# Performance work log

Measured on AMD Instinct MI355X. Metric: run time of the kernel, lower is better.

The kernel has to match this reference:

```python
import jax, jax.numpy as jnp
import numpy as np

N, E, D, H = 8192, 8, 2048, 2048


def setup_inputs() -> dict:
    key = jax.random.key(0)
    k1, k2, k3, k4 = jax.random.split(key, 4)
    x = jax.random.normal(k1, (N, D), dtype=jnp.float32)
    indices = jax.random.randint(k2, (N, 1), 0, E)  # top_k=1 expert assignment
    W = jax.random.normal(k3, (E, D, H), dtype=jnp.float32) * 0.02
    b = jax.random.normal(k4, (E, H), dtype=jnp.float32) * 0.02
    return {"x": x, "indices": indices, "W": W, "b": b}


def reference(x, indices, W, b):
    # Each token is routed to exactly one expert (top_k=1):
    # expert_id[n] = indices[n, 0]. The torch module loops experts e=0..E-1,
    # gathers tokens with (indices == e).any(-1) (ascending order via nonzero),
    # applies expert e's Linear + ReLU, and concatenates outputs in expert order.
    expert_id = indices[:, 0]                              # [N]
    # Dense dispatch: compute every expert's linear on every token, then pick
    # each token's own expert row (jit-friendly; no data-dependent shapes).
    y_all = jnp.einsum('nd,edh->neh', x, W) + b[None, :, :]  # [N, E, H]
    y = jnp.take_along_axis(y_all, expert_id[:, None, None], axis=1)[:, 1 - 1, :]  # [N, H]
    y = jax.nn.relu(y)
    # Concat in expert order == stable sort of tokens by expert id
    # (nonzero returns ascending indices, so within-expert order is preserved).
    order = jnp.argsort(expert_id)  # stable by default
    return y[order]
```

## Files before the change

kernel.cpp:

```cpp
#include <hip/hip_runtime.h>

#define N_TOK 8192
#define N_EXP 8
#define DIM   2048
#define HID   2048

typedef __attribute__((ext_vector_type(8))) short short8;
typedef __attribute__((ext_vector_type(4))) float f32x4;
typedef __attribute__((ext_vector_type(4))) unsigned short ushort4v;

__device__ inline unsigned short f2bf(float f) {
  unsigned int u = __builtin_bit_cast(unsigned int, f);
  unsigned int r = u + 0x7FFFu + ((u >> 16) & 1u);
  return (unsigned short)(r >> 16);
}

__global__ __launch_bounds__(256) void sort_experts(const int* __restrict__ idx,
                                                    int* __restrict__ perm,
                                                    int* __restrict__ offs) {
  __shared__ int cnt[256][8];
  __shared__ int base[8];
  const int t = threadIdx.x;
  int local[8] = {0,0,0,0,0,0,0,0};
  const int r0 = t * 32;
  for (int i = 0; i < 32; ++i) {
    int e = idx[r0 + i] & 7;
    ++local[e];
  }
#pragma unroll
  for (int e = 0; e < 8; ++e) cnt[t][e] = local[e];
  __syncthreads();
  if (t < 8) {
    int s = 0;
    for (int i = 0; i < 256; ++i) { int v = cnt[i][t]; cnt[i][t] = s; s += v; }
    base[t] = s;
  }
  __syncthreads();
  if (t == 0) {
    int s = 0;
    for (int e = 0; e < 8; ++e) { int v = base[e]; offs[e] = s; base[e] = s; s += v; }
    offs[8] = s;
  }
  __syncthreads();
  int pos[8];
#pragma unroll
  for (int e = 0; e < 8; ++e) pos[e] = base[e] + cnt[t][e];
  for (int i = 0; i < 32; ++i) {
    int r = r0 + i;
    int e = idx[r] & 7;
    perm[pos[e]++] = r;
  }
}

__global__ __launch_bounds__(256) void gather_convert_x(const float* __restrict__ x,
                                                        const int* __restrict__ perm,
                                                        unsigned short* __restrict__ xs) {
  int gid = blockIdx.x * 256 + threadIdx.x;
  int p = gid >> 8;
  int c = gid & 255;
  int src = perm[p];
  const float* sp = x + (size_t)src * DIM + c * 8;
  float4 a = *(const float4*)sp;
  float4 b = *(const float4*)(sp + 4);
  short8 o;
  o[0] = (short)f2bf(a.x); o[1] = (short)f2bf(a.y);
  o[2] = (short)f2bf(a.z); o[3] = (short)f2bf(a.w);
  o[4] = (short)f2bf(b.x); o[5] = (short)f2bf(b.y);
  o[6] = (short)f2bf(b.z); o[7] = (short)f2bf(b.w);
  *(short8*)(xs + (size_t)p * DIM + c * 8) = o;
}

__global__ __launch_bounds__(256) void transpose_convert_w(const float* __restrict__ W,
                                                           unsigned short* __restrict__ Wt) {
  __shared__ unsigned short tile[64][68];
  const int e = blockIdx.z;
  const int d0 = blockIdx.y * 64;
  const int h0 = blockIdx.x * 64;
  const int t = threadIdx.x;
  const int cr = t & 15;
  const int rr = t >> 4;
  const float* Wp = W + ((size_t)e * DIM + d0) * HID + h0;
#pragma unroll
  for (int i = 0; i < 4; ++i) {
    int d = rr + i * 16;
    float4 v = *(const float4*)(Wp + (size_t)d * HID + cr * 4);
    ushort4v o;
    o[0] = f2bf(v.x); o[1] = f2bf(v.y); o[2] = f2bf(v.z); o[3] = f2bf(v.w);
    *(ushort4v*)&tile[d][cr * 4] = o;
  }
  __syncthreads();
  unsigned short* op = Wt + ((size_t)e * HID + h0) * DIM + d0;
#pragma unroll
  for (int i = 0; i < 4; ++i) {
    int h = rr + i * 16;
    ushort4v o;
    o[0] = tile[cr * 4 + 0][h];
    o[1] = tile[cr * 4 + 1][h];
    o[2] = tile[cr * 4 + 2][h];
    o[3] = tile[cr * 4 + 3][h];
    *(ushort4v*)(op + (size_t)h * DIM + cr * 4) = o;
  }
}

#define NKT 32
#define SLOT_USH 24576

#define MM(D,A,B) D = __builtin_amdgcn_mfma_f32_16x16x32_bf16(A, B, D, 0, 0, 0)
#define GLD(SRC, DST) __builtin_amdgcn_global_load_lds( \
    (const __attribute__((address_space(1))) void*)(SRC), \
    (__attribute__((address_space(3))) void*)(DST), 16, 0, 0)
#define BAR() __builtin_amdgcn_s_barrier()
#define PRIO(x) __builtin_amdgcn_s_setprio(x)

__global__ __launch_bounds__(512, 2) void grouped_gemm(
    const unsigned short* __restrict__ xs,
    const unsigned short* __restrict__ Wt,
    const float* __restrict__ bias,
    const int* __restrict__ offs,
    float* __restrict__ out) {
  const int e   = blockIdx.z;
  const int off = offs[e];
  const int cnt = offs[e + 1] - off;
  const int mt  = blockIdx.y;
  if (mt * 128 >= cnt) return;
  const int n0 = blockIdx.x * 256;

  __shared__ __align__(16) unsigned short sm[3 * SLOT_USH];

  const int t    = threadIdx.x;
  const int lane = t & 63;
  const int wid  = t >> 6;
  const int wr   = wid >> 2;
  const int wc   = wid & 3;
  const int l15  = lane & 15;
  const int l4   = lane >> 4;

  const int cb0  = (l4 * 8) ^ ((l15 & 7) << 3);
  const int cb1  = cb0 ^ 32;
  const int arow = (wr * 64 + l15) * 64;
  const int brow = 8192 + (wc * 64 + l15) * 64;

  const int r0  = t >> 3;
  const int keu = ((t & 7) * 8) ^ ((r0 & 7) << 3);
  const int aBase = off + mt * 128;
  const int dA = t * 8;

  unsigned int pa0, pa1, pb0, pb1, pb2, pb3;
  {
    int p;
    p = aBase + 0 * 64 + r0; if (p > N_TOK - 1) p = N_TOK - 1; pa0 = (unsigned)p * 2048 + keu;
    p = aBase + 1 * 64 + r0; if (p > N_TOK - 1) p = N_TOK - 1; pa1 = (unsigned)p * 2048 + keu;
    unsigned int eW = (unsigned)e * (DIM * HID);
    pb0 = eW + (unsigned)(n0 + 0 * 64 + r0) * 2048 + keu;
    pb1 = eW + (unsigned)(n0 + 1 * 64 + r0) * 2048 + keu;
    pb2 = eW + (unsigned)(n0 + 2 * 64 + r0) * 2048 + keu;
    pb3 = eW + (unsigned)(n0 + 3 * 64 + r0) * 2048 + keu;
  }

#define ST_A(SBASE, KOFS) do { \
    GLD(xs + pa0 + (KOFS), sm + (SBASE) + 0 * 4096 + dA); \
    GLD(xs + pa1 + (KOFS), sm + (SBASE) + 1 * 4096 + dA); } while (0)
#define ST_B0(SBASE, KOFS) GLD(Wt + pb0 + (KOFS), sm + (SBASE) + 8192 + 0 * 4096 + dA)
#define ST_B123(SBASE, KOFS) do { \
    GLD(Wt + pb1 + (KOFS), sm + (SBASE) + 8192 + 1 * 4096 + dA); \
    GLD(Wt + pb2 + (KOFS), sm + (SBASE) + 8192 + 2 * 4096 + dA); \
    GLD(Wt + pb3 + (KOFS), sm + (SBASE) + 8192 + 3 * 4096 + dA); } while (0)

#define READ_FRAGS(SP, CB) \
    fa0 = *(const short8*)((SP) + arow + 0 * 1024 + (CB)); \
    fa1 = *(const short8*)((SP) + arow + 1 * 1024 + (CB)); \
    fa2 = *(const short8*)((SP) + arow + 2 * 1024 + (CB)); \
    fa3 = *(const short8*)((SP) + arow + 3 * 1024 + (CB)); \
    fb0 = *(const short8*)((SP) + brow + 0 * 1024 + (CB)); \
    fb1 = *(const short8*)((SP) + brow + 1 * 1024 + (CB)); \
    fb2 = *(const short8*)((SP) + brow + 2 * 1024 + (CB)); \
    fb3 = *(const short8*)((SP) + brow + 3 * 1024 + (CB));

#define MFMA16() \
    MM(acc[0][0],fa0,fb0); MM(acc[0][1],fa0,fb1); MM(acc[0][2],fa0,fb2); MM(acc[0][3],fa0,fb3); \
    MM(acc[1][0],fa1,fb0); MM(acc[1][1],fa1,fb1); MM(acc[1][2],fa1,fb2); MM(acc[1][3],fa1,fb3); \
    MM(acc[2][0],fa2,fb0); MM(acc[2][1],fa2,fb1); MM(acc[2][2],fa2,fb2); MM(acc[2][3],fa2,fb3); \
    MM(acc[3][0],fa3,fb0); MM(acc[3][1],fa3,fb1); MM(acc[3][2],fa3,fb2); MM(acc[3][3],fa3,fb3);

  f32x4 acc[4][4] = {};

  ST_A(0, 0); ST_B0(0, 0); ST_B123(0, 0);
  ST_A(SLOT_USH, 64); ST_B0(SLOT_USH, 64); ST_B123(SLOT_USH, 64);
  asm volatile("s_waitcnt vmcnt(6)" ::: "memory");
  BAR();

  short8 fa0, fa1, fa2, fa3, fb0, fb1, fb2, fb3;
  int sl = 0;
  int s2 = 2;

#pragma unroll 1
  for (int T = 0; T < NKT; ++T) {
    const unsigned short* SP = sm + sl * SLOT_USH;
    const int sb = s2 * SLOT_USH;
    const int kofs = (T + 2) * 64;
    const bool st = (T < NKT - 2);

    READ_FRAGS(SP, cb0);
    if (st) { ST_A(sb, kofs); ST_B0(sb, kofs); }
    BAR(); PRIO(1);
    MFMA16();
    PRIO(0); BAR();

    READ_FRAGS(SP, cb1);
    if (st) { ST_B123(sb, kofs); }
    BAR(); PRIO(1);
    MFMA16();
    PRIO(0);
    if (T < NKT - 2)       { asm volatile("s_waitcnt vmcnt(6)" ::: "memory"); }
    else if (T == NKT - 2) { asm volatile("s_waitcnt vmcnt(0)" ::: "memory"); }
    BAR();

    sl = (sl == 2) ? 0 : sl + 1;
    s2 = (s2 == 2) ? 0 : s2 + 1;
  }

#pragma unroll
  for (int n = 0; n < 4; ++n) {
    int col = n0 + wc * 64 + n * 16 + l15;
    float bv = bias[e * HID + col];
#pragma unroll
    for (int m = 0; m < 4; ++m) {
#pragma unroll
      for (int q = 0; q < 4; ++q) {
        int r = wr * 64 + m * 16 + l4 * 4 + q;
        if (mt * 128 + r < cnt) {
          float v = acc[m][n][q] + bv;
          out[(size_t)(off + mt * 128 + r) * HID + col] = v > 0.f ? v : 0.f;
        }
      }
    }
  }
}

extern "C" void kernel_launch(void* const* d_in, const int* in_sizes, int n_in,
                              void* d_out, int out_size, void* d_ws, size_t ws_size,
                              hipStream_t stream) {
  const float* x   = (const float*)d_in[0];
  const int*   idx = (const int*)d_in[1];
  const float* W   = (const float*)d_in[2];
  const float* b   = (const float*)d_in[3];
  float* out = (float*)d_out;

  char* ws = (char*)d_ws;
  unsigned short* xs = (unsigned short*)ws;
  unsigned short* Wt = (unsigned short*)(ws + (size_t)N_TOK * DIM * 2);
  int* perm = (int*)(ws + (size_t)N_TOK * DIM * 2 + (size_t)N_EXP * DIM * HID * 2);
  int* offs = perm + N_TOK;

  sort_experts<<<1, 256, 0, stream>>>(idx, perm, offs);
  gather_convert_x<<<N_TOK * (DIM / 8) / 256, 256, 0, stream>>>(x, perm, xs);
  transpose_convert_w<<<dim3(HID / 64, DIM / 64, N_EXP), 256, 0, stream>>>(W, Wt);
  grouped_gemm<<<dim3(HID / 256, N_TOK / 128, N_EXP), 512, 0, stream>>>(xs, Wt, b, offs, out);
}
```

Measured before the change: 182.6 us.

## Shrink GEMM tile to 128x128 with K=32 steps and 4-stage pipeline

Changes the grouped GEMM block tile from 128x256 with 512 threads to 128x128 with 256 threads, cutting each K step from 64 to 32 and moving from a 3-slot to a 4-slot LDS ring that loads three tiles ahead. The LDS swizzle and per-step load and MFMA schedule are rewritten to match. The aim is more blocks for better CU occupancy and less LDS per block. The cost is lower arithmetic intensity per loaded byte and twice as many barriers per K.

```diff
diff --git a/kernel.cpp b/kernel.cpp
--- a/kernel.cpp
+++ b/kernel.cpp
@@ -102,8 +102,8 @@
   }
 }
 
-#define NKT 32
-#define SLOT_USH 24576
+#define NKT 64
+#define SLOT 8192
 
 #define MM(D,A,B) D = __builtin_amdgcn_mfma_f32_16x16x32_bf16(A, B, D, 0, 0, 0)
 #define GLD(SRC, DST) __builtin_amdgcn_global_load_lds( \
@@ -112,7 +112,7 @@
 #define BAR() __builtin_amdgcn_s_barrier()
 #define PRIO(x) __builtin_amdgcn_s_setprio(x)
 
-__global__ __launch_bounds__(512, 2) void grouped_gemm(
+__global__ __launch_bounds__(256, 2) void grouped_gemm(
     const unsigned short* __restrict__ xs,
     const unsigned short* __restrict__ Wt,
     const float* __restrict__ bias,
@@ -123,29 +123,28 @@
   const int cnt = offs[e + 1] - off;
   const int mt  = blockIdx.y;
   if (mt * 128 >= cnt) return;
-  const int n0 = blockIdx.x * 256;
-
-  __shared__ __align__(16) unsigned short sm[3 * SLOT_USH];
+  const int n0 = blockIdx.x * 128;
+
+  __shared__ __align__(16) unsigned short sm[4 * SLOT];
 
   const int t    = threadIdx.x;
   const int lane = t & 63;
   const int wid  = t >> 6;
-  const int wr   = wid >> 2;
-  const int wc   = wid & 3;
+  const int wr   = wid >> 1;
+  const int wc   = wid & 1;
   const int l15  = lane & 15;
   const int l4   = lane >> 4;
 
-  const int cb0  = (l4 * 8) ^ ((l15 & 7) << 3);
-  const int cb1  = cb0 ^ 32;
-  const int arow = (wr * 64 + l15) * 64;
-  const int brow = 8192 + (wc * 64 + l15) * 64;
-
-  const int r0  = t >> 3;
-  const int keu = ((t & 7) * 8) ^ ((r0 & 7) << 3);
+  const int ksw = (l4 ^ (l15 & 3)) * 8;
+  const int arow = (wr * 64 + l15) * 32;
+  const int brow = 4096 + (wc * 64 + l15) * 32;
+
+  const int r0  = t >> 2;
+  const int keu = ((t & 3) ^ (r0 & 3)) * 8;
   const int aBase = off + mt * 128;
   const int dA = t * 8;
 
-  unsigned int pa0, pa1, pb0, pb1, pb2, pb3;
+  unsigned int pa0, pa1, pb0, pb1;
   {
     int p;
     p = aBase + 0 * 64 + r0; if (p > N_TOK - 1) p = N_TOK - 1; pa0 = (unsigned)p * 2048 + keu;
@@ -153,70 +152,49 @@
     unsigned int eW = (unsigned)e * (DIM * HID);
     pb0 = eW + (unsigned)(n0 + 0 * 64 + r0) * 2048 + keu;
     pb1 = eW + (unsigned)(n0 + 1 * 64 + r0) * 2048 + keu;
-    pb2 = eW + (unsigned)(n0 + 2 * 64 + r0) * 2048 + keu;
-    pb3 = eW + (unsigned)(n0 + 3 * 64 + r0) * 2048 + keu;
-  }
-
-#define ST_A(SBASE, KOFS) do { \
-    GLD(xs + pa0 + (KOFS), sm + (SBASE) + 0 * 4096 + dA); \
-    GLD(xs + pa1 + (KOFS), sm + (SBASE) + 1 * 4096 + dA); } while (0)
-#define ST_B0(SBASE, KOFS) GLD(Wt + pb0 + (KOFS), sm + (SBASE) + 8192 + 0 * 4096 + dA)
-#define ST_B123(SBASE, KOFS) do { \
-    GLD(Wt + pb1 + (KOFS), sm + (SBASE) + 8192 + 1 * 4096 + dA); \
-    GLD(Wt + pb2 + (KOFS), sm + (SBASE) + 8192 + 2 * 4096 + dA); \
-    GLD(Wt + pb3 + (KOFS), sm + (SBASE) + 8192 + 3 * 4096 + dA); } while (0)
-
-#define READ_FRAGS(SP, CB) \
-    fa0 = *(const short8*)((SP) + arow + 0 * 1024 + (CB)); \
-    fa1 = *(const short8*)((SP) + arow + 1 * 1024 + (CB)); \
-    fa2 = *(const short8*)((SP) + arow + 2 * 1024 + (CB)); \
-    fa3 = *(const short8*)((SP) + arow + 3 * 1024 + (CB)); \
-    fb0 = *(const short8*)((SP) + brow + 0 * 1024 + (CB)); \
-    fb1 = *(const short8*)((SP) + brow + 1 * 1024 + (CB)); \
-    fb2 = *(const short8*)((SP) + brow + 2 * 1024 + (CB)); \
-    fb3 = *(const short8*)((SP) + brow + 3 * 1024 + (CB));
-
-#define MFMA16() \
-    MM(acc[0][0],fa0,fb0); MM(acc[0][1],fa0,fb1); MM(acc[0][2],fa0,fb2); MM(acc[0][3],fa0,fb3); \
-    MM(acc[1][0],fa1,fb0); MM(acc[1][1],fa1,fb1); MM(acc[1][2],fa1,fb2); MM(acc[1][3],fa1,fb3); \
-    MM(acc[2][0],fa2,fb0); MM(acc[2][1],fa2,fb1); MM(acc[2][2],fa2,fb2); MM(acc[2][3],fa2,fb3); \
-    MM(acc[3][0],fa3,fb0); MM(acc[3][1],fa3,fb1); MM(acc[3][2],fa3,fb2); MM(acc[3][3],fa3,fb3);
+  }
+
+#define ST_TILE(SBASE, KOFS) do { \
+    GLD(xs + pa0 + (KOFS), sm + (SBASE) + 0 * 2048 + dA); \
+    GLD(xs + pa1 + (KOFS), sm + (SBASE) + 1 * 2048 + dA); \
+    GLD(Wt + pb0 + (KOFS), sm + (SBASE) + 4096 + 0 * 2048 + dA); \
+    GLD(Wt + pb1 + (KOFS), sm + (SBASE) + 4096 + 1 * 2048 + dA); } while (0)
 
   f32x4 acc[4][4] = {};
 
-  ST_A(0, 0); ST_B0(0, 0); ST_B123(0, 0);
-  ST_A(SLOT_USH, 64); ST_B0(SLOT_USH, 64); ST_B123(SLOT_USH, 64);
-  asm volatile("s_waitcnt vmcnt(6)" ::: "memory");
+  ST_TILE(0 * SLOT, 0);
+  ST_TILE(1 * SLOT, 32);
+  ST_TILE(2 * SLOT, 64);
+  asm volatile("s_waitcnt vmcnt(8)" ::: "memory");
   BAR();
 
   short8 fa0, fa1, fa2, fa3, fb0, fb1, fb2, fb3;
-  int sl = 0;
-  int s2 = 2;
 
 #pragma unroll 1
   for (int T = 0; T < NKT; ++T) {
-    const unsigned short* SP = sm + sl * SLOT_USH;
-    const int sb = s2 * SLOT_USH;
-    const int kofs = (T + 2) * 64;
-    const bool st = (T < NKT - 2);
-
-    READ_FRAGS(SP, cb0);
-    if (st) { ST_A(sb, kofs); ST_B0(sb, kofs); }
+    const unsigned short* SP = sm + (T & 3) * SLOT;
+
+    fa0 = *(const short8*)(SP + arow + 0 * 512 + ksw);
+    fa1 = *(const short8*)(SP + arow + 1 * 512 + ksw);
+    fa2 = *(const short8*)(SP + arow + 2 * 512 + ksw);
+    fa3 = *(const short8*)(SP + arow + 3 * 512 + ksw);
+    fb0 = *(const short8*)(SP + brow + 0 * 512 + ksw);
+    fb1 = *(const short8*)(SP + brow + 1 * 512 + ksw);
+    fb2 = *(const short8*)(SP + brow + 2 * 512 + ksw);
+    fb3 = *(const short8*)(SP + brow + 3 * 512 + ksw);
+
+    if (T < NKT - 3) ST_TILE(((T + 3) & 3) * SLOT, (T + 3) * 32);
+
     BAR(); PRIO(1);
-    MFMA16();
-    PRIO(0); BAR();
-
-    READ_FRAGS(SP, cb1);
-    if (st) { ST_B123(sb, kofs); }
-    BAR(); PRIO(1);
-    MFMA16();
+    MM(acc[0][0],fa0,fb0); MM(acc[0][1],fa0,fb1); MM(acc[0][2],fa0,fb2); MM(acc[0][3],fa0,fb3);
+    MM(acc[1][0],fa1,fb0); MM(acc[1][1],fa1,fb1); MM(acc[1][2],fa1,fb2); MM(acc[1][3],fa1,fb3);
+    MM(acc[2][0],fa2,fb0); MM(acc[2][1],fa2,fb1); MM(acc[2][2],fa2,fb2); MM(acc[2][3],fa2,fb3);
+    MM(acc[3][0],fa3,fb0); MM(acc[3][1],fa3,fb1); MM(acc[3][2],fa3,fb2); MM(acc[3][3],fa3,fb3);
     PRIO(0);
-    if (T < NKT - 2)       { asm volatile("s_waitcnt vmcnt(6)" ::: "memory"); }
+    if (T < NKT - 3)       { asm volatile("s_waitcnt vmcnt(8)" ::: "memory"); }
+    else if (T == NKT - 3) { asm volatile("s_waitcnt vmcnt(4)" ::: "memory"); }
     else if (T == NKT - 2) { asm volatile("s_waitcnt vmcnt(0)" ::: "memory"); }
     BAR();
-
-    sl = (sl == 2) ? 0 : sl + 1;
-    s2 = (s2 == 2) ? 0 : s2 + 1;
   }
 
 #pragma unroll
@@ -255,5 +233,5 @@
   sort_experts<<<1, 256, 0, stream>>>(idx, perm, offs);
   gather_convert_x<<<N_TOK * (DIM / 8) / 256, 256, 0, stream>>>(x, perm, xs);
   transpose_convert_w<<<dim3(HID / 64, DIM / 64, N_EXP), 256, 0, stream>>>(W, Wt);
-  grouped_gemm<<<dim3(HID / 256, N_TOK / 128, N_EXP), 512, 0, stream>>>(xs, Wt, b, offs, out);
-}
+  grouped_gemm<<<dim3(HID / 128, N_TOK / 128, N_EXP), 256, 0, stream>>>(xs, Wt, b, offs, out);
+}
```

Result: no change. 184.4 us (+1.0%).

## Use persistent job-list grouped GEMM with 256x128 tiles and merge prep kernels

Applied to the files above, without the earlier changes.

The sort kernel now also builds a compact list of (expert, m-tile) jobs, so the GEMM becomes a persistent 256-block kernel that loops only over real tiles instead of launching a full grid where many blocks exit early. The block tile changes from 128x256 to 256x128 (2x4 waves become 4x2), which alters the load split across the two half-stages. The x gather/convert and W transpose/convert kernels are merged into one launch to save a launch and let the two overlap. Risks include tail imbalance from the fixed 256-block stride and the extra indirection through the job list.

```diff
diff --git a/kernel.cpp b/kernel.cpp
--- a/kernel.cpp
+++ b/kernel.cpp
@@ -17,7 +17,8 @@
 
 __global__ __launch_bounds__(256) void sort_experts(const int* __restrict__ idx,
                                                     int* __restrict__ perm,
-                                                    int* __restrict__ offs) {
+                                                    int* __restrict__ offs,
+                                                    int* __restrict__ jobs) {
   __shared__ int cnt[256][8];
   __shared__ int base[8];
   const int t = threadIdx.x;
@@ -37,9 +38,15 @@
   }
   __syncthreads();
   if (t == 0) {
-    int s = 0;
-    for (int e = 0; e < 8; ++e) { int v = base[e]; offs[e] = s; base[e] = s; s += v; }
+    int s = 0, njm = 0;
+    for (int e = 0; e < 8; ++e) {
+      int v = base[e];
+      offs[e] = s; base[e] = s; s += v;
+      int nm = (v + 255) >> 8;
+      for (int mt = 0; mt < nm; ++mt) jobs[1 + njm++] = e | (mt << 8);
+    }
     offs[8] = s;
+    jobs[0] = njm;
   }
   __syncthreads();
   int pos[8];
@@ -52,58 +59,60 @@
   }
 }
 
-__global__ __launch_bounds__(256) void gather_convert_x(const float* __restrict__ x,
-                                                        const int* __restrict__ perm,
-                                                        unsigned short* __restrict__ xs) {
-  int gid = blockIdx.x * 256 + threadIdx.x;
-  int p = gid >> 8;
-  int c = gid & 255;
-  int src = perm[p];
-  const float* sp = x + (size_t)src * DIM + c * 8;
-  float4 a = *(const float4*)sp;
-  float4 b = *(const float4*)(sp + 4);
-  short8 o;
-  o[0] = (short)f2bf(a.x); o[1] = (short)f2bf(a.y);
-  o[2] = (short)f2bf(a.z); o[3] = (short)f2bf(a.w);
-  o[4] = (short)f2bf(b.x); o[5] = (short)f2bf(b.y);
-  o[6] = (short)f2bf(b.z); o[7] = (short)f2bf(b.w);
-  *(short8*)(xs + (size_t)p * DIM + c * 8) = o;
-}
-
-__global__ __launch_bounds__(256) void transpose_convert_w(const float* __restrict__ W,
-                                                           unsigned short* __restrict__ Wt) {
+__global__ __launch_bounds__(256) void prep(const float* __restrict__ x,
+                                            const int* __restrict__ perm,
+                                            unsigned short* __restrict__ xs,
+                                            const float* __restrict__ W,
+                                            unsigned short* __restrict__ Wt) {
   __shared__ unsigned short tile[64][68];
-  const int e = blockIdx.z;
-  const int d0 = blockIdx.y * 64;
-  const int h0 = blockIdx.x * 64;
   const int t = threadIdx.x;
-  const int cr = t & 15;
-  const int rr = t >> 4;
-  const float* Wp = W + ((size_t)e * DIM + d0) * HID + h0;
-#pragma unroll
-  for (int i = 0; i < 4; ++i) {
-    int d = rr + i * 16;
-    float4 v = *(const float4*)(Wp + (size_t)d * HID + cr * 4);
-    ushort4v o;
-    o[0] = f2bf(v.x); o[1] = f2bf(v.y); o[2] = f2bf(v.z); o[3] = f2bf(v.w);
-    *(ushort4v*)&tile[d][cr * 4] = o;
-  }
-  __syncthreads();
-  unsigned short* op = Wt + ((size_t)e * HID + h0) * DIM + d0;
-#pragma unroll
-  for (int i = 0; i < 4; ++i) {
-    int h = rr + i * 16;
-    ushort4v o;
-    o[0] = tile[cr * 4 + 0][h];
-    o[1] = tile[cr * 4 + 1][h];
-    o[2] = tile[cr * 4 + 2][h];
-    o[3] = tile[cr * 4 + 3][h];
-    *(ushort4v*)(op + (size_t)h * DIM + cr * 4) = o;
+  if (blockIdx.x < 8192) {
+    int gid = blockIdx.x * 256 + t;
+    int p = gid >> 8;
+    int c = gid & 255;
+    int src = perm[p];
+    const float* sp = x + (size_t)src * DIM + c * 8;
+    float4 a = *(const float4*)sp;
+    float4 b = *(const float4*)(sp + 4);
+    short8 o;
+    o[0] = (short)f2bf(a.x); o[1] = (short)f2bf(a.y);
+    o[2] = (short)f2bf(a.z); o[3] = (short)f2bf(a.w);
+    o[4] = (short)f2bf(b.x); o[5] = (short)f2bf(b.y);
+    o[6] = (short)f2bf(b.z); o[7] = (short)f2bf(b.w);
+    *(short8*)(xs + (size_t)p * DIM + c * 8) = o;
+  } else {
+    const int b = blockIdx.x - 8192;
+    const int e  = b >> 10;
+    const int d0 = ((b >> 5) & 31) * 64;
+    const int h0 = (b & 31) * 64;
+    const int cr = t & 15;
+    const int rr = t >> 4;
+    const float* Wp = W + ((size_t)e * DIM + d0) * HID + h0;
+#pragma unroll
+    for (int i = 0; i < 4; ++i) {
+      int d = rr + i * 16;
+      float4 v = *(const float4*)(Wp + (size_t)d * HID + cr * 4);
+      ushort4v o;
+      o[0] = f2bf(v.x); o[1] = f2bf(v.y); o[2] = f2bf(v.z); o[3] = f2bf(v.w);
+      *(ushort4v*)&tile[d][cr * 4] = o;
+    }
+    __syncthreads();
+    unsigned short* op = Wt + ((size_t)e * HID + h0) * DIM + d0;
+#pragma unroll
+    for (int i = 0; i < 4; ++i) {
+      int h = rr + i * 16;
+      ushort4v o;
+      o[0] = tile[cr * 4 + 0][h];
+      o[1] = tile[cr * 4 + 1][h];
+      o[2] = tile[cr * 4 + 2][h];
+      o[3] = tile[cr * 4 + 3][h];
+      *(ushort4v*)(op + (size_t)h * DIM + cr * 4) = o;
+    }
   }
 }
 
 #define NKT 32
-#define SLOT_USH 24576
+#define SLOT 24576
 
 #define MM(D,A,B) D = __builtin_amdgcn_mfma_f32_16x16x32_bf16(A, B, D, 0, 0, 0)
 #define GLD(SRC, DST) __builtin_amdgcn_global_load_lds( \
@@ -117,124 +126,138 @@
     const unsigned short* __restrict__ Wt,
     const float* __restrict__ bias,
     const int* __restrict__ offs,
+    const int* __restrict__ jobs,
     float* __restrict__ out) {
-  const int e   = blockIdx.z;
-  const int off = offs[e];
-  const int cnt = offs[e + 1] - off;
-  const int mt  = blockIdx.y;
-  if (mt * 128 >= cnt) return;
-  const int n0 = blockIdx.x * 256;
-
-  __shared__ __align__(16) unsigned short sm[3 * SLOT_USH];
+  __shared__ __align__(16) unsigned short sm[3 * SLOT];
 
   const int t    = threadIdx.x;
   const int lane = t & 63;
   const int wid  = t >> 6;
-  const int wr   = wid >> 2;
-  const int wc   = wid & 3;
+  const int wr   = wid >> 1;
+  const int wc   = wid & 1;
   const int l15  = lane & 15;
   const int l4   = lane >> 4;
 
   const int cb0  = (l4 * 8) ^ ((l15 & 7) << 3);
   const int cb1  = cb0 ^ 32;
   const int arow = (wr * 64 + l15) * 64;
-  const int brow = 8192 + (wc * 64 + l15) * 64;
+  const int brow = 16384 + (wc * 64 + l15) * 64;
 
   const int r0  = t >> 3;
   const int keu = ((t & 7) * 8) ^ ((r0 & 7) << 3);
-  const int aBase = off + mt * 128;
   const int dA = t * 8;
 
-  unsigned int pa0, pa1, pb0, pb1, pb2, pb3;
-  {
-    int p;
-    p = aBase + 0 * 64 + r0; if (p > N_TOK - 1) p = N_TOK - 1; pa0 = (unsigned)p * 2048 + keu;
-    p = aBase + 1 * 64 + r0; if (p > N_TOK - 1) p = N_TOK - 1; pa1 = (unsigned)p * 2048 + keu;
-    unsigned int eW = (unsigned)e * (DIM * HID);
-    pb0 = eW + (unsigned)(n0 + 0 * 64 + r0) * 2048 + keu;
-    pb1 = eW + (unsigned)(n0 + 1 * 64 + r0) * 2048 + keu;
-    pb2 = eW + (unsigned)(n0 + 2 * 64 + r0) * 2048 + keu;
-    pb3 = eW + (unsigned)(n0 + 3 * 64 + r0) * 2048 + keu;
-  }
-
-#define ST_A(SBASE, KOFS) do { \
+  const int njm   = jobs[0];
+  const int total = njm * 16;
+
+#pragma unroll 1
+  for (int idx = blockIdx.x; idx < total; idx += 256) {
+    const int jm  = jobs[1 + (idx >> 4)];
+    const int e   = jm & 255;
+    const int mt  = jm >> 8;
+    const int nx  = idx & 15;
+    const int off = offs[e];
+    const int cnt = offs[e + 1] - off;
+    const int aBase = off + mt * 256;
+    const int n0  = nx * 128;
+
+    unsigned int pa0, pa1, pa2, pa3, pb0, pb1;
+    {
+      int p;
+      p = aBase + 0 * 64 + r0; if (p > N_TOK - 1) p = N_TOK - 1; pa0 = (unsigned)p * 2048 + keu;
+      p = aBase + 1 * 64 + r0; if (p > N_TOK - 1) p = N_TOK - 1; pa1 = (unsigned)p * 2048 + keu;
+      p = aBase + 2 * 64 + r0; if (p > N_TOK - 1) p = N_TOK - 1; pa2 = (unsigned)p * 2048 + keu;
+      p = aBase + 3 * 64 + r0; if (p > N_TOK - 1) p = N_TOK - 1; pa3 = (unsigned)p * 2048 + keu;
+      unsigned int eW = (unsigned)e * (DIM * HID);
+      pb0 = eW + (unsigned)(n0 + 0 * 64 + r0) * 2048 + keu;
+      pb1 = eW + (unsigned)(n0 + 1 * 64 + r0) * 2048 + keu;
+    }
+
+#define ST_HALF1(SBASE, KOFS) do { \
     GLD(xs + pa0 + (KOFS), sm + (SBASE) + 0 * 4096 + dA); \
-    GLD(xs + pa1 + (KOFS), sm + (SBASE) + 1 * 4096 + dA); } while (0)
-#define ST_B0(SBASE, KOFS) GLD(Wt + pb0 + (KOFS), sm + (SBASE) + 8192 + 0 * 4096 + dA)
-#define ST_B123(SBASE, KOFS) do { \
-    GLD(Wt + pb1 + (KOFS), sm + (SBASE) + 8192 + 1 * 4096 + dA); \
-    GLD(Wt + pb2 + (KOFS), sm + (SBASE) + 8192 + 2 * 4096 + dA); \
-    GLD(Wt + pb3 + (KOFS), sm + (SBASE) + 8192 + 3 * 4096 + dA); } while (0)
-
-#define READ_FRAGS(SP, CB) \
-    fa0 = *(const short8*)((SP) + arow + 0 * 1024 + (CB)); \
-    fa1 = *(const short8*)((SP) + arow + 1 * 1024 + (CB)); \
-    fa2 = *(const short8*)((SP) + arow + 2 * 1024 + (CB)); \
-    fa3 = *(const short8*)((SP) + arow + 3 * 1024 + (CB)); \
-    fb0 = *(const short8*)((SP) + brow + 0 * 1024 + (CB)); \
-    fb1 = *(const short8*)((SP) + brow + 1 * 1024 + (CB)); \
-    fb2 = *(const short8*)((SP) + brow + 2 * 1024 + (CB)); \
-    fb3 = *(const short8*)((SP) + brow + 3 * 1024 + (CB));
-
-#define MFMA16() \
-    MM(acc[0][0],fa0,fb0); MM(acc[0][1],fa0,fb1); MM(acc[0][2],fa0,fb2); MM(acc[0][3],fa0,fb3); \
-    MM(acc[1][0],fa1,fb0); MM(acc[1][1],fa1,fb1); MM(acc[1][2],fa1,fb2); MM(acc[1][3],fa1,fb3); \
-    MM(acc[2][0],fa2,fb0); MM(acc[2][1],fa2,fb1); MM(acc[2][2],fa2,fb2); MM(acc[2][3],fa2,fb3); \
-    MM(acc[3][0],fa3,fb0); MM(acc[3][1],fa3,fb1); MM(acc[3][2],fa3,fb2); MM(acc[3][3],fa3,fb3);
-
-  f32x4 acc[4][4] = {};
-
-  ST_A(0, 0); ST_B0(0, 0); ST_B123(0, 0);
-  ST_A(SLOT_USH, 64); ST_B0(SLOT_USH, 64); ST_B123(SLOT_USH, 64);
-  asm volatile("s_waitcnt vmcnt(6)" ::: "memory");
-  BAR();
-
-  short8 fa0, fa1, fa2, fa3, fb0, fb1, fb2, fb3;
-  int sl = 0;
-  int s2 = 2;
+    GLD(xs + pa1 + (KOFS), sm + (SBASE) + 1 * 4096 + dA); \
+    GLD(xs + pa2 + (KOFS), sm + (SBASE) + 2 * 4096 + dA); } while (0)
+#define ST_HALF2(SBASE, KOFS) do { \
+    GLD(xs + pa3 + (KOFS), sm + (SBASE) + 3 * 4096 + dA); \
+    GLD(Wt + pb0 + (KOFS), sm + (SBASE) + 16384 + 0 * 4096 + dA); \
+    GLD(Wt + pb1 + (KOFS), sm + (SBASE) + 16384 + 1 * 4096 + dA); } while (0)
+
+    f32x4 acc[4][4] = {};
+
+    ST_HALF1(0, 0);        ST_HALF2(0, 0);
+    ST_HALF1(SLOT, 64);    ST_HALF2(SLOT, 64);
+    asm volatile("s_waitcnt vmcnt(6)" ::: "memory");
+    BAR();
+
+    short8 fa0, fa1, fa2, fa3, fb0, fb1, fb2, fb3;
+    int sl = 0;
+    int s2 = 2;
 
 #pragma unroll 1
-  for (int T = 0; T < NKT; ++T) {
-    const unsigned short* SP = sm + sl * SLOT_USH;
-    const int sb = s2 * SLOT_USH;
-    const int kofs = (T + 2) * 64;
-    const bool st = (T < NKT - 2);
-
-    READ_FRAGS(SP, cb0);
-    if (st) { ST_A(sb, kofs); ST_B0(sb, kofs); }
-    BAR(); PRIO(1);
-    MFMA16();
-    PRIO(0); BAR();
-
-    READ_FRAGS(SP, cb1);
-    if (st) { ST_B123(sb, kofs); }
-    BAR(); PRIO(1);
-    MFMA16();
-    PRIO(0);
-    if (T < NKT - 2)       { asm volatile("s_waitcnt vmcnt(6)" ::: "memory"); }
-    else if (T == NKT - 2) { asm volatile("s_waitcnt vmcnt(0)" ::: "memory"); }
-    BAR();
-
-    sl = (sl == 2) ? 0 : sl + 1;
-    s2 = (s2 == 2) ? 0 : s2 + 1;
-  }
-
-#pragma unroll
-  for (int n = 0; n < 4; ++n) {
-    int col = n0 + wc * 64 + n * 16 + l15;
-    float bv = bias[e * HID + col];
-#pragma unroll
-    for (int m = 0; m < 4; ++m) {
-#pragma unroll
-      for (int q = 0; q < 4; ++q) {
-        int r = wr * 64 + m * 16 + l4 * 4 + q;
-        if (mt * 128 + r < cnt) {
-          float v = acc[m][n][q] + bv;
-          out[(size_t)(off + mt * 128 + r) * HID + col] = v > 0.f ? v : 0.f;
+    for (int T = 0; T < NKT; ++T) {
+      const unsigned short* SP = sm + sl * SLOT;
+      const int sb = s2 * SLOT;
+      const int kofs = (T + 2) * 64;
+      const bool st = (T < NKT - 2);
+
+      fa0 = *(const short8*)(SP + arow + 0 * 1024 + cb0);
+      fa1 = *(const short8*)(SP + arow + 1 * 1024 + cb0);
+      fa2 = *(const short8*)(SP + arow + 2 * 1024 + cb0);
+      fa3 = *(const short8*)(SP + arow + 3 * 1024 + cb0);
+      fb0 = *(const short8*)(SP + brow + 0 * 1024 + cb0);
+      fb1 = *(const short8*)(SP + brow + 1 * 1024 + cb0);
+      fb2 = *(const short8*)(SP + brow + 2 * 1024 + cb0);
+      fb3 = *(const short8*)(SP + brow + 3 * 1024 + cb0);
+      if (st) ST_HALF1(sb, kofs);
+      BAR(); PRIO(1);
+      MM(acc[0][0],fa0,fb0); MM(acc[0][1],fa0,fb1); MM(acc[0][2],fa0,fb2); MM(acc[0][3],fa0,fb3);
+      MM(acc[1][0],fa1,fb0); MM(acc[1][1],fa1,fb1); MM(acc[1][2],fa1,fb2); MM(acc[1][3],fa1,fb3);
+      MM(acc[2][0],fa2,fb0); MM(acc[2][1],fa2,fb1); MM(acc[2][2],fa2,fb2); MM(acc[2][3],fa2,fb3);
+      MM(acc[3][0],fa3,fb0); MM(acc[3][1],fa3,fb1); MM(acc[3][2],fa3,fb2); MM(acc[3][3],fa3,fb3);
+      PRIO(0); BAR();
+
+      fa0 = *(const short8*)(SP + arow + 0 * 1024 + cb1);
+      fa1 = *(const short8*)(SP + arow + 1 * 1024 + cb1);
+      fa2 = *(const short8*)(SP + arow + 2 * 1024 + cb1);
+      fa3 = *(const short8*)(SP + arow + 3 * 1024 + cb1);
+      fb0 = *(const short8*)(SP + brow + 0 * 1024 + cb1);
+      fb1 = *(const short8*)(SP + brow + 1 * 1024 + cb1);
+      fb2 = *(const short8*)(SP + brow + 2 * 1024 + cb1);
+      fb3 = *(const short8*)(SP + brow + 3 * 1024 + cb1);
+      if (st) ST_HALF2(sb, kofs);
+      BAR(); PRIO(1);
+      MM(acc[0][0],fa0,fb0); MM(acc[0][1],fa0,fb1); MM(acc[0][2],fa0,fb2); MM(acc[0][3],fa0,fb3);
+      MM(acc[1][0],fa1,fb0); MM(acc[1][1],fa1,fb1); MM(acc[1][2],fa1,fb2); MM(acc[1][3],fa1,fb3);
+      MM(acc[2][0],fa2,fb0); MM(acc[2][1],fa2,fb1); MM(acc[2][2],fa2,fb2); MM(acc[2][3],fa2,fb3);
+      MM(acc[3][0],fa3,fb0); MM(acc[3][1],fa3,fb1); MM(acc[3][2],fa3,fb2); MM(acc[3][3],fa3,fb3);
+      PRIO(0);
+      if (T < NKT - 2)       { asm volatile("s_waitcnt vmcnt(6)" ::: "memory"); }
+      else if (T == NKT - 2) { asm volatile("s_waitcnt vmcnt(0)" ::: "memory"); }
+      BAR();
+
+      sl = (sl == 2) ? 0 : sl + 1;
+      s2 = (s2 == 2) ? 0 : s2 + 1;
+    }
+
+#pragma unroll
+    for (int n = 0; n < 4; ++n) {
+      int col = n0 + wc * 64 + n * 16 + l15;
+      float bv = bias[e * HID + col];
+#pragma unroll
+      for (int m = 0; m < 4; ++m) {
+#pragma unroll
+        for (int q = 0; q < 4; ++q) {
+          int r = wr * 64 + m * 16 + l4 * 4 + q;
+          if (mt * 256 + r < cnt) {
+            float v = acc[m][n][q] + bv;
+            out[(size_t)(off + mt * 256 + r) * HID + col] = v > 0.f ? v : 0.f;
+          }
         }
       }
     }
   }
+#undef ST_HALF1
+#undef ST_HALF2
 }
 
 extern "C" void kernel_launch(void* const* d_in, const int* in_sizes, int n_in,
@@ -251,9 +274,9 @@
   unsigned short* Wt = (unsigned short*)(ws + (size_t)N_TOK * DIM * 2);
   int* perm = (int*)(ws + (size_t)N_TOK * DIM * 2 + (size_t)N_EXP * DIM * HID * 2);
   int* offs = perm + N_TOK;
-
-  sort_experts<<<1, 256, 0, stream>>>(idx, perm, offs);
-  gather_convert_x<<<N_TOK * (DIM / 8) / 256, 256, 0, stream>>>(x, perm, xs);
-  transpose_convert_w<<<dim3(HID / 64, DIM / 64, N_EXP), 256, 0, stream>>>(W, Wt);
-  grouped_gemm<<<dim3(HID / 256, N_TOK / 128, N_EXP), 512, 0, stream>>>(xs, Wt, b, offs, out);
-}
+  int* jobs = offs + 16;
+
+  sort_experts<<<1, 256, 0, stream>>>(idx, perm, offs, jobs);
+  prep<<<16384, 256, 0, stream>>>(x, perm, xs, W, Wt);
+  grouped_gemm<<<256, 512, 0, stream>>>(xs, Wt, b, offs, jobs, out);
+}
```

After: 188.8 us. 1.03x slower.

## Fuse weight conversion into persistent grouped GEMM with compact job list

Applied to the files above, without the earlier changes.

Removes the separate transpose/convert pass for W by loading fp32 weights directly in the GEMM, converting them to bf16 in registers and writing them transposed into LDS. It also switches to a persistent grid of 256 blocks walking a compact job list built during the sort, with 256x128 tiles and double buffering. This avoids writing and re-reading a bf16 copy of W and skips launching empty tiles. In exchange, the GEMM reads fp32 weights with scalar strided loads per expert M-tile and puts conversion work and register pressure on the main loop.

```diff
diff --git a/kernel.cpp b/kernel.cpp
--- a/kernel.cpp
+++ b/kernel.cpp
@@ -7,7 +7,6 @@
 
 typedef __attribute__((ext_vector_type(8))) short short8;
 typedef __attribute__((ext_vector_type(4))) float f32x4;
-typedef __attribute__((ext_vector_type(4))) unsigned short ushort4v;
 
 __device__ inline unsigned short f2bf(float f) {
   unsigned int u = __builtin_bit_cast(unsigned int, f);
@@ -17,7 +16,8 @@
 
 __global__ __launch_bounds__(256) void sort_experts(const int* __restrict__ idx,
                                                     int* __restrict__ perm,
-                                                    int* __restrict__ offs) {
+                                                    int* __restrict__ offs,
+                                                    int* __restrict__ jobs) {
   __shared__ int cnt[256][8];
   __shared__ int base[8];
   const int t = threadIdx.x;
@@ -37,9 +37,15 @@
   }
   __syncthreads();
   if (t == 0) {
-    int s = 0;
-    for (int e = 0; e < 8; ++e) { int v = base[e]; offs[e] = s; base[e] = s; s += v; }
+    int s = 0, njm = 0;
+    for (int e = 0; e < 8; ++e) {
+      int v = base[e];
+      offs[e] = s; base[e] = s; s += v;
+      int nm = (v + 255) >> 8;
+      for (int mt = 0; mt < nm; ++mt) jobs[1 + njm++] = e | (mt << 8);
+    }
     offs[8] = s;
+    jobs[0] = njm;
   }
   __syncthreads();
   int pos[8];
@@ -52,9 +58,9 @@
   }
 }
 
-__global__ __launch_bounds__(256) void gather_convert_x(const float* __restrict__ x,
-                                                        const int* __restrict__ perm,
-                                                        unsigned short* __restrict__ xs) {
+__global__ __launch_bounds__(256) void prep_x(const float* __restrict__ x,
+                                              const int* __restrict__ perm,
+                                              unsigned short* __restrict__ xs) {
   int gid = blockIdx.x * 256 + threadIdx.x;
   int p = gid >> 8;
   int c = gid & 255;
@@ -70,40 +76,8 @@
   *(short8*)(xs + (size_t)p * DIM + c * 8) = o;
 }
 
-__global__ __launch_bounds__(256) void transpose_convert_w(const float* __restrict__ W,
-                                                           unsigned short* __restrict__ Wt) {
-  __shared__ unsigned short tile[64][68];
-  const int e = blockIdx.z;
-  const int d0 = blockIdx.y * 64;
-  const int h0 = blockIdx.x * 64;
-  const int t = threadIdx.x;
-  const int cr = t & 15;
-  const int rr = t >> 4;
-  const float* Wp = W + ((size_t)e * DIM + d0) * HID + h0;
-#pragma unroll
-  for (int i = 0; i < 4; ++i) {
-    int d = rr + i * 16;
-    float4 v = *(const float4*)(Wp + (size_t)d * HID + cr * 4);
-    ushort4v o;
-    o[0] = f2bf(v.x); o[1] = f2bf(v.y); o[2] = f2bf(v.z); o[3] = f2bf(v.w);
-    *(ushort4v*)&tile[d][cr * 4] = o;
-  }
-  __syncthreads();
-  unsigned short* op = Wt + ((size_t)e * HID + h0) * DIM + d0;
-#pragma unroll
-  for (int i = 0; i < 4; ++i) {
-    int h = rr + i * 16;
-    ushort4v o;
-    o[0] = tile[cr * 4 + 0][h];
-    o[1] = tile[cr * 4 + 1][h];
-    o[2] = tile[cr * 4 + 2][h];
-    o[3] = tile[cr * 4 + 3][h];
-    *(ushort4v*)(op + (size_t)h * DIM + cr * 4) = o;
-  }
-}
-
 #define NKT 32
-#define SLOT_USH 24576
+#define SLOT 24576
 
 #define MM(D,A,B) D = __builtin_amdgcn_mfma_f32_16x16x32_bf16(A, B, D, 0, 0, 0)
 #define GLD(SRC, DST) __builtin_amdgcn_global_load_lds( \
@@ -114,59 +88,64 @@
 
 __global__ __launch_bounds__(512, 2) void grouped_gemm(
     const unsigned short* __restrict__ xs,
-    const unsigned short* __restrict__ Wt,
+    const float* __restrict__ W,
     const float* __restrict__ bias,
     const int* __restrict__ offs,
+    const int* __restrict__ jobs,
     float* __restrict__ out) {
-  const int e   = blockIdx.z;
-  const int off = offs[e];
-  const int cnt = offs[e + 1] - off;
-  const int mt  = blockIdx.y;
-  if (mt * 128 >= cnt) return;
-  const int n0 = blockIdx.x * 256;
-
-  __shared__ __align__(16) unsigned short sm[3 * SLOT_USH];
+  __shared__ __align__(16) unsigned short sm[2 * SLOT];
 
   const int t    = threadIdx.x;
   const int lane = t & 63;
   const int wid  = t >> 6;
-  const int wr   = wid >> 2;
-  const int wc   = wid & 3;
+  const int wr   = wid >> 1;
+  const int wc   = wid & 1;
   const int l15  = lane & 15;
   const int l4   = lane >> 4;
 
   const int cb0  = (l4 * 8) ^ ((l15 & 7) << 3);
   const int cb1  = cb0 ^ 32;
   const int arow = (wr * 64 + l15) * 64;
-  const int brow = 8192 + (wc * 64 + l15) * 64;
+  const int brow = 16384 + (wc * 64 + l15) * 64;
 
   const int r0  = t >> 3;
   const int keu = ((t & 7) * 8) ^ ((r0 & 7) << 3);
-  const int aBase = off + mt * 128;
-  const int dA = t * 8;
-
-  unsigned int pa0, pa1, pb0, pb1, pb2, pb3;
-  {
-    int p;
-    p = aBase + 0 * 64 + r0; if (p > N_TOK - 1) p = N_TOK - 1; pa0 = (unsigned)p * 2048 + keu;
-    p = aBase + 1 * 64 + r0; if (p > N_TOK - 1) p = N_TOK - 1; pa1 = (unsigned)p * 2048 + keu;
-    unsigned int eW = (unsigned)e * (DIM * HID);
-    pb0 = eW + (unsigned)(n0 + 0 * 64 + r0) * 2048 + keu;
-    pb1 = eW + (unsigned)(n0 + 1 * 64 + r0) * 2048 + keu;
-    pb2 = eW + (unsigned)(n0 + 2 * 64 + r0) * 2048 + keu;
-    pb3 = eW + (unsigned)(n0 + 3 * 64 + r0) * 2048 + keu;
-  }
+  const int dA  = t * 8;
+
+  const int h    = t & 127;
+  const int dgrp = t >> 7;
+  const int bw0  = 16384 + h * 64 + ((dgrp * 16) ^ ((h & 7) << 3));
+  const int bw1  = 16384 + h * 64 + ((dgrp * 16 + 8) ^ ((h & 7) << 3));
+
+#define LDB(P, K0) do { unsigned bi_ = bB + (unsigned)(K0) * 2048u; \
+    P##0  = W[bi_];            P##1  = W[bi_ + 2048u]; \
+    P##2  = W[bi_ + 4096u];    P##3  = W[bi_ + 6144u]; \
+    P##4  = W[bi_ + 8192u];    P##5  = W[bi_ + 10240u]; \
+    P##6  = W[bi_ + 12288u];   P##7  = W[bi_ + 14336u]; \
+    P##8  = W[bi_ + 16384u];   P##9  = W[bi_ + 18432u]; \
+    P##10 = W[bi_ + 20480u];   P##11 = W[bi_ + 22528u]; \
+    P##12 = W[bi_ + 24576u];   P##13 = W[bi_ + 26624u]; \
+    P##14 = W[bi_ + 28672u];   P##15 = W[bi_ + 30720u]; } while (0)
+
+#define CVW(P, NSBASE) do { short8 s0_, s1_; \
+    s0_[0]=(short)f2bf(P##0);  s0_[1]=(short)f2bf(P##1); \
+    s0_[2]=(short)f2bf(P##2);  s0_[3]=(short)f2bf(P##3); \
+    s0_[4]=(short)f2bf(P##4);  s0_[5]=(short)f2bf(P##5); \
+    s0_[6]=(short)f2bf(P##6);  s0_[7]=(short)f2bf(P##7); \
+    s1_[0]=(short)f2bf(P##8);  s1_[1]=(short)f2bf(P##9); \
+    s1_[2]=(short)f2bf(P##10); s1_[3]=(short)f2bf(P##11); \
+    s1_[4]=(short)f2bf(P##12); s1_[5]=(short)f2bf(P##13); \
+    s1_[6]=(short)f2bf(P##14); s1_[7]=(short)f2bf(P##15); \
+    *(short8*)(sm + (NSBASE) + bw0) = s0_; \
+    *(short8*)(sm + (NSBASE) + bw1) = s1_; } while (0)
 
 #define ST_A(SBASE, KOFS) do { \
     GLD(xs + pa0 + (KOFS), sm + (SBASE) + 0 * 4096 + dA); \
-    GLD(xs + pa1 + (KOFS), sm + (SBASE) + 1 * 4096 + dA); } while (0)
-#define ST_B0(SBASE, KOFS) GLD(Wt + pb0 + (KOFS), sm + (SBASE) + 8192 + 0 * 4096 + dA)
-#define ST_B123(SBASE, KOFS) do { \
-    GLD(Wt + pb1 + (KOFS), sm + (SBASE) + 8192 + 1 * 4096 + dA); \
-    GLD(Wt + pb2 + (KOFS), sm + (SBASE) + 8192 + 2 * 4096 + dA); \
-    GLD(Wt + pb3 + (KOFS), sm + (SBASE) + 8192 + 3 * 4096 + dA); } while (0)
-
-#define READ_FRAGS(SP, CB) \
+    GLD(xs + pa1 + (KOFS), sm + (SBASE) + 1 * 4096 + dA); \
+    GLD(xs + pa2 + (KOFS), sm + (SBASE) + 2 * 4096 + dA); \
+    GLD(xs + pa3 + (KOFS), sm + (SBASE) + 3 * 4096 + dA); } while (0)
+
+#define READF(SP, CB) \
     fa0 = *(const short8*)((SP) + arow + 0 * 1024 + (CB)); \
     fa1 = *(const short8*)((SP) + arow + 1 * 1024 + (CB)); \
     fa2 = *(const short8*)((SP) + arow + 2 * 1024 + (CB)); \
@@ -182,55 +161,89 @@
     MM(acc[2][0],fa2,fb0); MM(acc[2][1],fa2,fb1); MM(acc[2][2],fa2,fb2); MM(acc[2][3],fa2,fb3); \
     MM(acc[3][0],fa3,fb0); MM(acc[3][1],fa3,fb1); MM(acc[3][2],fa3,fb2); MM(acc[3][3],fa3,fb3);
 
-  f32x4 acc[4][4] = {};
-
-  ST_A(0, 0); ST_B0(0, 0); ST_B123(0, 0);
-  ST_A(SLOT_USH, 64); ST_B0(SLOT_USH, 64); ST_B123(SLOT_USH, 64);
-  asm volatile("s_waitcnt vmcnt(6)" ::: "memory");
-  BAR();
-
-  short8 fa0, fa1, fa2, fa3, fb0, fb1, fb2, fb3;
-  int sl = 0;
-  int s2 = 2;
+#define ITER(T, LB, CB) { \
+    const int T_ = (T); \
+    const unsigned short* SP = sm + ((T_ & 1) ? SLOT : 0); \
+    const int NS = (T_ & 1) ? 0 : SLOT; \
+    READF(SP, cb0); \
+    if (T_ < NKT - 1) ST_A(NS, (T_ + 1) * 64); \
+    if (T_ < NKT - 2) LDB(LB, (T_ + 2) * 64); \
+    __builtin_amdgcn_sched_barrier(0); \
+    BAR(); PRIO(1); \
+    MFMA16(); \
+    PRIO(0); BAR(); \
+    READF(SP, cb1); \
+    if (T_ < NKT - 1) CVW(CB, NS); \
+    BAR(); PRIO(1); \
+    MFMA16(); \
+    PRIO(0); \
+    if (T_ < NKT - 2)       { asm volatile("s_waitcnt vmcnt(16) lgkmcnt(0)" ::: "memory"); } \
+    else if (T_ == NKT - 2) { asm volatile("s_waitcnt vmcnt(0) lgkmcnt(0)" ::: "memory"); } \
+    else                    { asm volatile("s_waitcnt lgkmcnt(0)" ::: "memory"); } \
+    BAR(); \
+  }
+
+  const int total = jobs[0] * 16;
 
 #pragma unroll 1
-  for (int T = 0; T < NKT; ++T) {
-    const unsigned short* SP = sm + sl * SLOT_USH;
-    const int sb = s2 * SLOT_USH;
-    const int kofs = (T + 2) * 64;
-    const bool st = (T < NKT - 2);
-
-    READ_FRAGS(SP, cb0);
-    if (st) { ST_A(sb, kofs); ST_B0(sb, kofs); }
-    BAR(); PRIO(1);
-    MFMA16();
-    PRIO(0); BAR();
-
-    READ_FRAGS(SP, cb1);
-    if (st) { ST_B123(sb, kofs); }
-    BAR(); PRIO(1);
-    MFMA16();
-    PRIO(0);
-    if (T < NKT - 2)       { asm volatile("s_waitcnt vmcnt(6)" ::: "memory"); }
-    else if (T == NKT - 2) { asm volatile("s_waitcnt vmcnt(0)" ::: "memory"); }
+  for (int j = blockIdx.x; j < total; j += 256) {
+    const int jm  = jobs[1 + (j >> 4)];
+    const int e   = jm & 255;
+    const int mt  = jm >> 8;
+    const int nx  = j & 15;
+    const int off = offs[e];
+    const int cnt = offs[e + 1] - off;
+    if (mt * 256 >= cnt) continue;
+    const int aBase = off + mt * 256;
+    const int n0  = nx * 128;
+
+    unsigned int pa0, pa1, pa2, pa3;
+    {
+      int p;
+      p = aBase + 0 * 64 + r0; if (p > N_TOK - 1) p = N_TOK - 1; pa0 = (unsigned)p * 2048 + keu;
+      p = aBase + 1 * 64 + r0; if (p > N_TOK - 1) p = N_TOK - 1; pa1 = (unsigned)p * 2048 + keu;
+      p = aBase + 2 * 64 + r0; if (p > N_TOK - 1) p = N_TOK - 1; pa2 = (unsigned)p * 2048 + keu;
+      p = aBase + 3 * 64 + r0; if (p > N_TOK - 1) p = N_TOK - 1; pa3 = (unsigned)p * 2048 + keu;
+    }
+    const unsigned int bB = (unsigned)e * 4194304u + (unsigned)(n0 + h)
+                          + (unsigned)dgrp * 32768u;
+
+    float brA0, brA1, brA2, brA3, brA4, brA5, brA6, brA7,
+          brA8, brA9, brA10, brA11, brA12, brA13, brA14, brA15;
+    float brB0, brB1, brB2, brB3, brB4, brB5, brB6, brB7,
+          brB8, brB9, brB10, brB11, brB12, brB13, brB14, brB15;
+
+    f32x4 acc[4][4] = {};
+
+    ST_A(0, 0);
+    LDB(brA, 0);
+    asm volatile("s_waitcnt vmcnt(0)" ::: "memory");
+    CVW(brA, 0);
+    LDB(brB, 64);
+    asm volatile("s_waitcnt lgkmcnt(0)" ::: "memory");
     BAR();
 
-    sl = (sl == 2) ? 0 : sl + 1;
-    s2 = (s2 == 2) ? 0 : s2 + 1;
-  }
-
-#pragma unroll
-  for (int n = 0; n < 4; ++n) {
-    int col = n0 + wc * 64 + n * 16 + l15;
-    float bv = bias[e * HID + col];
-#pragma unroll
-    for (int m = 0; m < 4; ++m) {
-#pragma unroll
-      for (int q = 0; q < 4; ++q) {
-        int r = wr * 64 + m * 16 + l4 * 4 + q;
-        if (mt * 128 + r < cnt) {
-          float v = acc[m][n][q] + bv;
-          out[(size_t)(off + mt * 128 + r) * HID + col] = v > 0.f ? v : 0.f;
+    short8 fa0, fa1, fa2, fa3, fb0, fb1, fb2, fb3;
+
+#pragma unroll 1
+    for (int tt = 0; tt < NKT; tt += 2) {
+      ITER(tt,     brA, brB);
+      ITER(tt + 1, brB, brA);
+    }
+
+#pragma unroll
+    for (int n = 0; n < 4; ++n) {
+      int col = n0 + wc * 64 + n * 16 + l15;
+      float bv = bias[e * HID + col];
+#pragma unroll
+      for (int m = 0; m < 4; ++m) {
+#pragma unroll
+        for (int q = 0; q < 4; ++q) {
+          int r = wr * 64 + m * 16 + l4 * 4 + q;
+          if (mt * 256 + r < cnt) {
+            float v = acc[m][n][q] + bv;
+            out[(size_t)(off + mt * 256 + r) * HID + col] = v > 0.f ? v : 0.f;
+          }
         }
       }
     }
@@ -248,12 +261,11 @@
 
   char* ws = (char*)d_ws;
   unsigned short* xs = (unsigned short*)ws;
-  unsigned short* Wt = (unsigned short*)(ws + (size_t)N_TOK * DIM * 2);
-  int* perm = (int*)(ws + (size_t)N_TOK * DIM * 2 + (size_t)N_EXP * DIM * HID * 2);
+  int* perm = (int*)(ws + (size_t)N_TOK * DIM * 2);
   int* offs = perm + N_TOK;
-
-  sort_experts<<<1, 256, 0, stream>>>(idx, perm, offs);
-  gather_convert_x<<<N_TOK * (DIM / 8) / 256, 256, 0, stream>>>(x, perm, xs);
-  transpose_convert_w<<<dim3(HID / 64, DIM / 64, N_EXP), 256, 0, stream>>>(W, Wt);
-  grouped_gemm<<<dim3(HID / 256, N_TOK / 128, N_EXP), 512, 0, stream>>>(xs, Wt, b, offs, out);
-}
+  int* jobs = offs + 16;
+
+  sort_experts<<<1, 256, 0, stream>>>(idx, perm, offs, jobs);
+  prep_x<<<N_TOK * (DIM / 8) / 256, 256, 0, stream>>>(x, perm, xs);
+  grouped_gemm<<<256, 512, 0, stream>>>(xs, W, b, offs, jobs, out);
+}
```

Result: slower. 210.8 us (+15.4%).
